# Performance work log

Hardware: AMD Instinct MI355X
Metric: run time of the kernel (lower is better)

## Reference

```python
import jax, jax.numpy as jnp
import numpy as np

B, D, N, H = 2, 1024, 2048, 16
Da = D // H
NEG = -1e30


def setup_inputs() -> dict:
    key = jax.random.key(0)
    k1, k2, k3, k4, k5 = jax.random.split(key, 5)
    x = jax.random.normal(k1, (B, D, N), dtype=jnp.float32)
    mask = jnp.ones((B, N), dtype=jnp.float32)
    s = 1.0 / np.sqrt(D)
    Wq = jax.random.normal(k2, (H, D, Da), dtype=jnp.float32) * s
    Wk = jax.random.normal(k3, (H, D, Da), dtype=jnp.float32) * s
    Wv = jax.random.normal(k4, (H, D, Da), dtype=jnp.float32) * s
    Wo = jax.random.normal(k5, (D, D), dtype=jnp.float32) * s
    return {"x": x, "mask": mask, "Wq": Wq, "Wk": Wk, "Wv": Wv, "Wo": Wo}


def reference(x, mask, Wq, Wk, Wv, Wo):
    # x: [B, D, N] -> [B, N, D]
    xt = jnp.swapaxes(x, 1, 2)
    scale = 1.0 / np.sqrt(Da)
    # per-head projections, batched over heads: [B, H, N, Da]
    q = jnp.einsum("bnd,hde->bhne", xt, Wq)
    k = jnp.einsum("bnd,hde->bhne", xt, Wk)
    v = jnp.einsum("bnd,hde->bhne", xt, Wv)
    # scaled scores: [B, H, N, N]
    scores = jnp.einsum("bhne,bhme->bhnm", q, k) * scale
    hmask = mask[:, None, None, :]  # additive mask over keys
    vmask = mask[:, None, :, None]  # multiplicative mask over queries
    scores = scores * hmask + (1.0 - hmask) * NEG
    attn = jax.nn.softmax(scores, axis=-1) * vmask
    heads = jnp.einsum("bhnm,bhme->bhne", attn, v)
    # concat heads along feature dim: [B, N, H*Da]
    head = jnp.swapaxes(heads, 1, 2).reshape(xt.shape[0], xt.shape[1], H * Da)
    out = head @ Wo  # [B, N, D]
    return jnp.swapaxes(out, 1, 2)  # [B, D, N]
```

## Files before the change

### kernel.cpp

```cpp
#include <hip/hip_runtime.h>

typedef _Float16 f16;
typedef _Float16 f16x4 __attribute__((ext_vector_type(4)));
typedef _Float16 f16x8 __attribute__((ext_vector_type(8)));
typedef __fp16 fp16x2 __attribute__((ext_vector_type(2)));
typedef float f32x4 __attribute__((ext_vector_type(4)));
typedef float f32x16 __attribute__((ext_vector_type(16)));
typedef int i32x4 __attribute__((ext_vector_type(4)));

#define NEGV (-1e30f)

#if __has_builtin(__builtin_amdgcn_exp2f)
#define EXP2(x) __builtin_amdgcn_exp2f(x)
#else
#define EXP2(x) exp2f(x)
#endif

__device__ __forceinline__ void gload16(const f16* g, f16* l) {
  __builtin_amdgcn_global_load_lds(
      (const __attribute__((address_space(1))) void*)g,
      (__attribute__((address_space(3))) void*)l, 16, 0, 0);
}

__device__ __forceinline__ int pkh(float a, float b) {
  fp16x2 p = __builtin_amdgcn_cvt_pkrtz(a, b);
  return __builtin_bit_cast(int, p);
}

__device__ __forceinline__ void plswap(int& a, int& b) {
#if __has_builtin(__builtin_amdgcn_permlane32_swap)
  auto r = __builtin_amdgcn_permlane32_swap(a, b, false, false);
  a = r[0];
  b = r[1];
#else
  int an = __shfl_xor(b, 32);
  int bn = __shfl_xor(a, 32);
  bool lo = (threadIdx.x & 63) < 32;
  int a2 = lo ? a : an;
  int b2 = lo ? bn : b;
  a = a2;
  b = b2;
#endif
}

__global__ __launch_bounds__(256) void prep_kernel(
    const float* __restrict__ x, const float* __restrict__ Wq,
    const float* __restrict__ Wk, const float* __restrict__ Wv,
    const float* __restrict__ Wo, f16* __restrict__ xt,
    f16* __restrict__ WqkvT, f16* __restrict__ WoT)
{
  __shared__ float t[32][33];
  int tx = threadIdx.x & 31, ty = threadIdx.x >> 5;
  int id = blockIdx.x;
  const float* src;
  f16* dst;
  int a0, b0, sld;
  float sc = 1.0f;
  if (id < 4096) {
    int b = id >> 11, rem = id & 2047;
    a0 = (rem >> 6) * 32;
    b0 = (rem & 63) * 32;
    sld = 2048;
    src = x + (size_t)b * 1024 * 2048;
    dst = xt + (size_t)b * 2048 * 1024;
  } else if (id < 7168) {
    int i = id - 4096;
    a0 = (i & 31) * 32;
    b0 = ((i >> 5) & 1) * 32;
    int z = i >> 6, m = z >> 4, h = z & 15;
    sld = 64;
    src = ((m == 0) ? Wq : (m == 1) ? Wk : Wv) + (size_t)h * 65536;
    sc = (m == 0) ? 0.18033688011112042f : 1.0f;
    dst = WqkvT + (size_t)(m * 1024 + h * 64) * 1024;
  } else {
    int i = id - 7168;
    a0 = (i >> 5) * 32;
    b0 = (i & 31) * 32;
    sld = 1024;
    src = Wo;
    dst = WoT;
  }
#pragma unroll
  for (int i = 0; i < 4; ++i)
    t[ty + 8 * i][tx] = src[(size_t)(a0 + ty + 8 * i) * sld + b0 + tx] * sc;
  __syncthreads();
#pragma unroll
  for (int i = 0; i < 4; ++i)
    dst[(size_t)(b0 + ty + 8 * i) * 1024 + a0 + tx] = (f16)t[tx][ty + 8 * i];
}

__global__ __launch_bounds__(512, 4) void gemm_f16_kernel(
    const f16* __restrict__ A, const f16* __restrict__ Bt,
    int K, int ldc, long bstride, long cstride,
    f16* __restrict__ Ch, float* __restrict__ Cf,
    const float* __restrict__ rowmask, int mcol0,
    f16* __restrict__ Vt)
{
  __shared__ __align__(16) f16 smem[8192];
  f16* As = smem;
  f16* Bs = smem + 4096;

  int tid = threadIdx.x;
  int lane = tid & 63, w = tid >> 6, g = lane >> 4, r = lane & 15;
  int wr = w >> 2, wc = w & 3;

  int nbx = gridDim.x;
  int n = nbx * gridDim.y;
  int flat = blockIdx.y * nbx + blockIdx.x;
  int nf = (flat & 7) * (n >> 3) + (flat >> 3);
  int bx = nf % nbx, by = nf / nbx;

  size_t row0 = (size_t)by * 128;
  size_t col0 = (size_t)bx * 128;
  Bt += (size_t)blockIdx.z * (size_t)bstride;

  int srow = lane >> 2;
  int sseg = (lane & 3) * 8;

  f32x4 acc[4][2];
#pragma unroll
  for (int m = 0; m < 4; ++m)
#pragma unroll
    for (int nn = 0; nn < 2; ++nn)
      acc[m][nn] = (f32x4){0.f, 0.f, 0.f, 0.f};

  const f16* Ap = A + (row0 + w * 16 + srow) * (size_t)K + sseg;
  const f16* Bp = Bt + (col0 + w * 16 + srow) * (size_t)K + sseg;

  for (int k0 = 0; k0 < K; k0 += 32) {
    __syncthreads();
    gload16(Ap + k0, As + w * 512);
    gload16(Bp + k0, Bs + w * 512);
    __syncthreads();
    f16x8 af[4], bf[2];
#pragma unroll
    for (int m = 0; m < 4; ++m)
      af[m] = *(const f16x8*)&As[(wr * 64 + m * 16 + r) * 32 + g * 8];
#pragma unroll
    for (int nn = 0; nn < 2; ++nn)
      bf[nn] = *(const f16x8*)&Bs[(wc * 32 + nn * 16 + r) * 32 + g * 8];
#pragma unroll
    for (int m = 0; m < 4; ++m)
#pragma unroll
      for (int nn = 0; nn < 2; ++nn)
        acc[m][nn] = __builtin_amdgcn_mfma_f32_16x16x32_f16(af[m], bf[nn], acc[m][nn], 0, 0, 0);
  }

  if (Vt && col0 >= 2048) {
    int b = (int)(row0 >> 11);
    int n0 = (int)(row0 & 2047);
    int vcol0 = (int)col0 - 2048;
    __syncthreads();
#pragma unroll
    for (int h2 = 0; h2 < 2; ++h2) {
      if ((wc >> 1) == h2) {
        int wcl = wc & 1;
#pragma unroll
        for (int m = 0; m < 4; ++m)
#pragma unroll
          for (int nn = 0; nn < 2; ++nn) {
            int cl = wcl * 32 + nn * 16 + r;
            int row = wr * 64 + m * 16 + g * 4;
            int rowp = row ^ ((cl & 7) << 3);
            f16x4 v4 = {(f16)acc[m][nn][0], (f16)acc[m][nn][1],
                        (f16)acc[m][nn][2], (f16)acc[m][nn][3]};
            *(f16x4*)&smem[cl * 128 + rowp] = v4;
          }
      }
      __syncthreads();
#pragma unroll
      for (int ii = 0; ii < 2; ++ii) {
        int chunk = ii * 512 + tid;
        int el = chunk >> 4, seg = chunk & 15;
        int rowp = (seg * 8) ^ ((el & 7) << 3);
        f16x8 v8 = *(const f16x8*)&smem[el * 128 + rowp];
        *(f16x8*)&Vt[(size_t)(b * 1024 + vcol0 + h2 * 64 + el) * 2048 + n0 + seg * 8] = v8;
      }
      __syncthreads();
    }
  } else if (Ch) {
    Ch += (size_t)blockIdx.z * (size_t)cstride;
#pragma unroll
    for (int m = 0; m < 4; ++m)
#pragma unroll
      for (int nn = 0; nn < 2; ++nn)
#pragma unroll
        for (int q = 0; q < 4; ++q) {
          size_t row = row0 + wr * 64 + m * 16 + g * 4 + q;
          int col = (int)col0 + wc * 32 + nn * 16 + r;
          float v = acc[m][nn][q];
          if (rowmask && col >= mcol0) v *= rowmask[row];
          Ch[row * (size_t)ldc + col] = (f16)v;
        }
  } else {
    Cf += (size_t)blockIdx.z * (size_t)cstride;
#pragma unroll
    for (int m = 0; m < 4; ++m)
#pragma unroll
      for (int nn = 0; nn < 2; ++nn)
#pragma unroll
        for (int q = 0; q < 4; ++q)
          Cf[(row0 + wr * 64 + m * 16 + g * 4 + q) * (size_t)ldc +
             col0 + wc * 32 + nn * 16 + r] = acc[m][nn][q];
  }
}

__global__ __launch_bounds__(512, 4) void attn_kernel(const f16* __restrict__ qk,
                                                      const f16* __restrict__ Vt,
                                                      const float* __restrict__ mask,
                                                      f16* __restrict__ head)
{
  __shared__ __align__(16) f16 smem[16384];
  __shared__ __align__(16) float negc[2048];
  __shared__ __align__(16) float rl[8][32];
  __shared__ __align__(16) float mm[8][32];
  __shared__ __align__(16) float ll[8][32];
  __shared__ __align__(16) float aa[8][32];
  __shared__ __align__(16) float il[4][32];
  __shared__ int aflag;

  int tid = threadIdx.x;
  int w = tid >> 6, lane = tid & 63;
  int l31 = lane & 31, hb = lane >> 5;
  int hb4 = hb * 4;
  int wq = w >> 1, wk = w & 1;

  int flat = blockIdx.x;
  int nf = (flat & 7) * 64 + (flat >> 3);
  int qt = nf & 15, bh = nf >> 4;
  int b = bh >> 4, hh = bh & 15;
  const float* maskb = mask + b * 2048;

  if (tid == 0) aflag = 0;

  int qrow = qt * 128 + wq * 32 + l31;
  const f16* qp = qk + ((size_t)(b * 2048 + qrow)) * 2048 + hh * 64;
  f16x8 qf[4];
#pragma unroll
  for (int ec = 0; ec < 4; ++ec)
    qf[ec] = *(const f16x8*)(qp + ec * 16 + hb * 8);

  const f16* kg0 = qk + ((size_t)(b * 2048)) * 2048 + 1024 + hh * 64;
  const f16* vg0 = Vt + ((size_t)((b * 16 + hh) * 64)) * 2048;

  int srow = tid >> 3;
  int sseg = tid & 7;
  int s2 = (sseg ^ (srow & 7)) * 8;

  auto stage = [&](int nb, int kt_) {
    const f16* kg = kg0 + (size_t)kt_ * 64 * 2048;
    const f16* vg = vg0 + kt_ * 64;
    gload16(kg + (size_t)srow * 2048 + s2, smem + nb * 4096 + w * 512);
    gload16(vg + (size_t)srow * 2048 + s2, smem + 8192 + nb * 4096 + w * 512);
  };

  stage(0, 0);
  __syncthreads();

  {
    const float* mp = maskb + tid * 4;
    f32x4 m0 = *(const f32x4*)(mp);
    int localany = 0;
#pragma unroll
    for (int j = 0; j < 4; ++j) {
      negc[tid * 4 + j] = (1.0f - m0[j]) * NEGV;
      localany |= (m0[j] != 1.0f);
    }
    if (localany) aflag = 1;
  }
  __syncthreads();
  const bool anymask = (aflag != 0);

  f32x16 o0, o1;
#pragma unroll
  for (int i = 0; i < 16; ++i) { o0[i] = 0.f; o1[i] = 0.f; }
  float mrun = -INFINITY, lrun = 0.f;

  int krow = wk * 32 + l31;
  int kb = krow * 64;
  int k7 = krow & 7;
  int vk7 = l31 & 7;
  int vb0 = l31 * 64, vb1 = vb0 + 2048;

  for (int kt = 0; kt < 32; ++kt) {
    int cur = kt & 1;
    if (kt + 1 < 32) stage(cur ^ 1, kt + 1);

    const f16* Kc = smem + cur * 4096;
    const f16* Vc = smem + 8192 + cur * 4096;

    f32x16 s;
    if (anymask) {
      const float* nb = &negc[kt * 64 + wk * 32];
#pragma unroll
      for (int rr = 0; rr < 4; ++rr) {
        f32x4 cv = *(const f32x4*)&nb[rr * 8 + hb4];
#pragma unroll
        for (int j = 0; j < 4; ++j) s[rr * 4 + j] = cv[j];
      }
    } else {
#pragma unroll
      for (int i = 0; i < 16; ++i) s[i] = 0.f;
    }
    __builtin_amdgcn_s_setprio(1);
#pragma unroll
    for (int ec = 0; ec < 4; ++ec) {
      int so = ((((ec << 1) | hb) ^ k7) << 3);
      f16x8 kf = *(const f16x8*)&Kc[kb + so];
      s = __builtin_amdgcn_mfma_f32_32x32x16_f16(kf, qf[ec], s, 0, 0, 0);
    }
    __builtin_amdgcn_s_setprio(0);

    float a[16];
#pragma unroll
    for (int i = 0; i < 16; ++i) a[i] = s[i];
#pragma unroll
    for (int stp = 8; stp > 0; stp >>= 1)
#pragma unroll
      for (int i = 0; i < stp; ++i) a[i] = fmaxf(a[i], a[i + stp]);
    float pmax = fmaxf(a[0], __shfl_xor(a[0], 32));

    if (!__all(pmax - mrun <= 8.0f)) {
      float mnew = fmaxf(mrun, pmax);
      float resc = EXP2(mrun - mnew);
      mrun = mnew;
      lrun *= resc;
      if (hb == 0) rl[w][l31] = resc;
#pragma unroll
      for (int rr = 0; rr < 4; ++rr) {
        f32x4 rv = *(const f32x4*)&rl[w][rr * 8 + hb4];
#pragma unroll
        for (int j = 0; j < 4; ++j) {
          o0[rr * 4 + j] *= rv[j];
          o1[rr * 4 + j] *= rv[j];
        }
      }
    }

    float p[16];
#pragma unroll
    for (int i = 0; i < 16; ++i) p[i] = EXP2(s[i] - mrun);
    float b2[8];
#pragma unroll
    for (int i = 0; i < 8; ++i) b2[i] = p[i] + p[i + 8];
#pragma unroll
    for (int stp = 4; stp > 0; stp >>= 1)
#pragma unroll
      for (int i = 0; i < stp; ++i) b2[i] += b2[i + stp];
    lrun += b2[0] + __shfl_xor(b2[0], 32);

    __builtin_amdgcn_s_setprio(1);
#pragma unroll
    for (int kc = 0; kc < 2; ++kc) {
      int t0a = pkh(p[kc * 8 + 0], p[kc * 8 + 1]);
      int t0b = pkh(p[kc * 8 + 2], p[kc * 8 + 3]);
      int t1a = pkh(p[kc * 8 + 4], p[kc * 8 + 5]);
      int t1b = pkh(p[kc * 8 + 6], p[kc * 8 + 7]);
      plswap(t0a, t1a);
      plswap(t0b, t1b);
      f16x8 af = __builtin_bit_cast(f16x8, (i32x4){t0a, t0b, t1a, t1b});
      int vs = (((wk * 4 + (kc << 1)) | hb) ^ vk7) << 3;
      f16x8 vf0 = *(const f16x8*)&Vc[vb0 + vs];
      f16x8 vf1 = *(const f16x8*)&Vc[vb1 + vs];
      o0 = __builtin_amdgcn_mfma_f32_32x32x16_f16(af, vf0, o0, 0, 0, 0);
      o1 = __builtin_amdgcn_mfma_f32_32x32x16_f16(af, vf1, o1, 0, 0, 0);
    }
    __builtin_amdgcn_s_setprio(0);

    __syncthreads();
  }

  if (hb == 0) {
    mm[w][l31] = mrun;
    ll[w][l31] = lrun;
  }
  __syncthreads();
  {
    float mo = mm[w ^ 1][l31], lo = ll[w ^ 1][l31];
    float mt = fmaxf(mrun, mo);
    float a_self = EXP2(mrun - mt);
    float a_oth = EXP2(mo - mt);
    float lt = lrun * a_self + lo * a_oth;
    if (hb == 0) {
      aa[w][l31] = a_self;
      if (wk == 0) il[wq][l31] = maskb[qrow] / lt;
    }
  }
#pragma unroll
  for (int rr = 0; rr < 4; ++rr) {
    f32x4 av = *(const f32x4*)&aa[w][rr * 8 + hb4];
#pragma unroll
    for (int j = 0; j < 4; ++j) {
      o0[rr * 4 + j] *= av[j];
      o1[rr * 4 + j] *= av[j];
    }
  }
  float* scr = (float*)smem;
  if (wk == 1) {
    float* sp = scr + wq * 2048;
#pragma unroll
    for (int i = 0; i < 16; ++i) {
      sp[i * 64 + lane] = o0[i];
      sp[(16 + i) * 64 + lane] = o1[i];
    }
  }
  __syncthreads();
  if (wk == 0) {
    float* sp = scr + wq * 2048;
#pragma unroll
    for (int i = 0; i < 16; ++i) {
      o0[i] += sp[i * 64 + lane];
      o1[i] += sp[(16 + i) * 64 + lane];
    }
    f16* hp = head + ((size_t)(b * 2048 + qt * 128 + wq * 32)) * 1024 + hh * 64 + l31;
#pragma unroll
    for (int rr = 0; rr < 4; ++rr) {
      f32x4 iv = *(const f32x4*)&il[wq][rr * 8 + hb4];
#pragma unroll
      for (int j = 0; j < 4; ++j) {
        int crow = j + rr * 8 + hb4;
        hp[(size_t)crow * 1024] = (f16)(o0[rr * 4 + j] * iv[j]);
        hp[(size_t)crow * 1024 + 32] = (f16)(o1[rr * 4 + j] * iv[j]);
      }
    }
  }
}

extern "C" void kernel_launch(void* const* d_in, const int* in_sizes, int n_in,
                              void* d_out, int out_size, void* d_ws, size_t ws_size,
                              hipStream_t stream)
{
  const float* x    = (const float*)d_in[0];
  const float* mask = (const float*)d_in[1];
  const float* Wq   = (const float*)d_in[2];
  const float* Wk   = (const float*)d_in[3];
  const float* Wv   = (const float*)d_in[4];
  const float* Wo   = (const float*)d_in[5];
  float* out = (float*)d_out;

  char* ws = (char*)d_ws;
  f16* xt_head = (f16*)(ws);
  f16* WqkvT   = (f16*)(ws + 8388608);
  f16* WoT     = (f16*)(ws + 14680064);
  f16* qk      = (f16*)(ws + 16777216);
  f16* Vt      = (f16*)(ws + 33554432);

  prep_kernel<<<dim3(8192), 256, 0, stream>>>(x, Wq, Wk, Wv, Wo, xt_head, WqkvT, WoT);

  gemm_f16_kernel<<<dim3(24, 32, 1), 512, 0, stream>>>(
      xt_head, WqkvT, 1024, 2048, 0, 0, qk, nullptr, mask, 1024, Vt);

  attn_kernel<<<dim3(512), 512, 0, stream>>>(qk, Vt, mask, xt_head);

  gemm_f16_kernel<<<dim3(16, 8, 2), 512, 0, stream>>>(
      WoT, xt_head, 1024, 2048, (long)2048 * 1024, (long)1024 * 2048, nullptr, out,
      nullptr, 0, nullptr);
}
```

Before: 132.5 us.

## Double attention key tile to 128 and use narrower tiles for output GEMM

The attention kernel now stages 128 keys per iteration instead of 64, doubling the shared K/V buffers and computing two score tiles per wave before one softmax update. This halves the loop trip count and the block barriers, at the cost of more LDS and registers per block, which can lower occupancy. The output-projection GEMM is templated to a 64-wide column tile, doubling the grid to 512 blocks for better CU coverage. A barrier is added before the final rescale step.

```diff
diff --git a/kernel.cpp b/kernel.cpp
--- a/kernel.cpp
+++ b/kernel.cpp
@@ -89,6 +89,7 @@
     dst[(size_t)(b0 + ty + 8 * i) * 1024 + a0 + tx] = (f16)t[tx][ty + 8 * i];
 }
 
+template <int BN>
 __global__ __launch_bounds__(512, 4) void gemm_f16_kernel(
     const f16* __restrict__ A, const f16* __restrict__ Bt,
     int K, int ldc, long bstride, long cstride,
@@ -96,6 +97,7 @@
     const float* __restrict__ rowmask, int mcol0,
     f16* __restrict__ Vt)
 {
+  const int NACC = BN / 64;
   __shared__ __align__(16) f16 smem[8192];
   f16* As = smem;
   f16* Bs = smem + 4096;
@@ -111,17 +113,17 @@
   int bx = nf % nbx, by = nf / nbx;
 
   size_t row0 = (size_t)by * 128;
-  size_t col0 = (size_t)bx * 128;
+  size_t col0 = (size_t)bx * BN;
   Bt += (size_t)blockIdx.z * (size_t)bstride;
 
   int srow = lane >> 2;
   int sseg = (lane & 3) * 8;
 
-  f32x4 acc[4][2];
+  f32x4 acc[4][NACC];
 #pragma unroll
   for (int m = 0; m < 4; ++m)
 #pragma unroll
-    for (int nn = 0; nn < 2; ++nn)
+    for (int nn = 0; nn < NACC; ++nn)
       acc[m][nn] = (f32x4){0.f, 0.f, 0.f, 0.f};
 
   const f16* Ap = A + (row0 + w * 16 + srow) * (size_t)K + sseg;
@@ -130,23 +132,23 @@
   for (int k0 = 0; k0 < K; k0 += 32) {
     __syncthreads();
     gload16(Ap + k0, As + w * 512);
-    gload16(Bp + k0, Bs + w * 512);
+    if (BN == 128 || w < 4) gload16(Bp + k0, Bs + w * 512);
     __syncthreads();
-    f16x8 af[4], bf[2];
+    f16x8 af[4], bf[NACC];
 #pragma unroll
     for (int m = 0; m < 4; ++m)
       af[m] = *(const f16x8*)&As[(wr * 64 + m * 16 + r) * 32 + g * 8];
 #pragma unroll
-    for (int nn = 0; nn < 2; ++nn)
-      bf[nn] = *(const f16x8*)&Bs[(wc * 32 + nn * 16 + r) * 32 + g * 8];
+    for (int nn = 0; nn < NACC; ++nn)
+      bf[nn] = *(const f16x8*)&Bs[(wc * (16 * NACC) + nn * 16 + r) * 32 + g * 8];
 #pragma unroll
     for (int m = 0; m < 4; ++m)
 #pragma unroll
-      for (int nn = 0; nn < 2; ++nn)
+      for (int nn = 0; nn < NACC; ++nn)
         acc[m][nn] = __builtin_amdgcn_mfma_f32_16x16x32_f16(af[m], bf[nn], acc[m][nn], 0, 0, 0);
   }
 
-  if (Vt && col0 >= 2048) {
+  if (BN == 128 && Vt && col0 >= 2048) {
     int b = (int)(row0 >> 11);
     int n0 = (int)(row0 & 2047);
     int vcol0 = (int)col0 - 2048;
@@ -158,7 +160,7 @@
 #pragma unroll
         for (int m = 0; m < 4; ++m)
 #pragma unroll
-          for (int nn = 0; nn < 2; ++nn) {
+          for (int nn = 0; nn < NACC; ++nn) {
             int cl = wcl * 32 + nn * 16 + r;
             int row = wr * 64 + m * 16 + g * 4;
             int rowp = row ^ ((cl & 7) << 3);
@@ -183,11 +185,11 @@
 #pragma unroll
     for (int m = 0; m < 4; ++m)
 #pragma unroll
-      for (int nn = 0; nn < 2; ++nn)
+      for (int nn = 0; nn < NACC; ++nn)
 #pragma unroll
         for (int q = 0; q < 4; ++q) {
           size_t row = row0 + wr * 64 + m * 16 + g * 4 + q;
-          int col = (int)col0 + wc * 32 + nn * 16 + r;
+          int col = (int)col0 + wc * (16 * NACC) + nn * 16 + r;
           float v = acc[m][nn][q];
           if (rowmask && col >= mcol0) v *= rowmask[row];
           Ch[row * (size_t)ldc + col] = (f16)v;
@@ -197,11 +199,11 @@
 #pragma unroll
     for (int m = 0; m < 4; ++m)
 #pragma unroll
-      for (int nn = 0; nn < 2; ++nn)
+      for (int nn = 0; nn < NACC; ++nn)
 #pragma unroll
         for (int q = 0; q < 4; ++q)
           Cf[(row0 + wr * 64 + m * 16 + g * 4 + q) * (size_t)ldc +
-             col0 + wc * 32 + nn * 16 + r] = acc[m][nn][q];
+             col0 + wc * (16 * NACC) + nn * 16 + r] = acc[m][nn][q];
   }
 }
 
@@ -210,7 +212,7 @@
                                                       const float* __restrict__ mask,
                                                       f16* __restrict__ head)
 {
-  __shared__ __align__(16) f16 smem[16384];
+  __shared__ __align__(16) f16 smem[32768];
   __shared__ __align__(16) float negc[2048];
   __shared__ __align__(16) float rl[8][32];
   __shared__ __align__(16) float mm[8][32];
@@ -243,15 +245,20 @@
   const f16* kg0 = qk + ((size_t)(b * 2048)) * 2048 + 1024 + hh * 64;
   const f16* vg0 = Vt + ((size_t)((b * 16 + hh) * 64)) * 2048;
 
-  int srow = tid >> 3;
-  int sseg = tid & 7;
-  int s2 = (sseg ^ (srow & 7)) * 8;
+  int ksrow = tid >> 3, kseg = tid & 7;
+  int ks2 = (kseg ^ (ksrow & 7)) * 8;
+  int vsrow = tid >> 4, vseg2 = tid & 15;
+  int vs2 = (vseg2 ^ (vsrow & 7)) * 8;
 
   auto stage = [&](int nb, int kt_) {
-    const f16* kg = kg0 + (size_t)kt_ * 64 * 2048;
-    const f16* vg = vg0 + kt_ * 64;
-    gload16(kg + (size_t)srow * 2048 + s2, smem + nb * 4096 + w * 512);
-    gload16(vg + (size_t)srow * 2048 + s2, smem + 8192 + nb * 4096 + w * 512);
+    const f16* kg = kg0 + (size_t)kt_ * 128 * 2048;
+    const f16* vg = vg0 + kt_ * 128;
+    f16* Kd = smem + nb * 8192;
+    f16* Vd = smem + 16384 + nb * 8192;
+    gload16(kg + (size_t)ksrow * 2048 + ks2, Kd + w * 512);
+    gload16(kg + (size_t)(ksrow + 64) * 2048 + ks2, Kd + 4096 + w * 512);
+    gload16(vg + (size_t)vsrow * 2048 + vs2, Vd + w * 512);
+    gload16(vg + (size_t)(vsrow + 32) * 2048 + vs2, Vd + 4096 + w * 512);
   };
 
   stage(0, 0);
@@ -276,44 +283,49 @@
   for (int i = 0; i < 16; ++i) { o0[i] = 0.f; o1[i] = 0.f; }
   float mrun = -INFINITY, lrun = 0.f;
 
-  int krow = wk * 32 + l31;
-  int kb = krow * 64;
-  int k7 = krow & 7;
-  int vk7 = l31 & 7;
-  int vb0 = l31 * 64, vb1 = vb0 + 2048;
-
-  for (int kt = 0; kt < 32; ++kt) {
+  int kb0 = (wk * 64 + l31) * 64;
+  int kb1 = kb0 + 2048;
+  int k7 = l31 & 7;
+  int vb0 = l31 * 128, vb1 = vb0 + 4096;
+
+  for (int kt = 0; kt < 16; ++kt) {
     int cur = kt & 1;
-    if (kt + 1 < 32) stage(cur ^ 1, kt + 1);
-
-    const f16* Kc = smem + cur * 4096;
-    const f16* Vc = smem + 8192 + cur * 4096;
-
-    f32x16 s;
+    if (kt + 1 < 16) stage(cur ^ 1, kt + 1);
+
+    const f16* Kc = smem + cur * 8192;
+    const f16* Vc = smem + 16384 + cur * 8192;
+
+    f32x16 s0, s1;
     if (anymask) {
-      const float* nb = &negc[kt * 64 + wk * 32];
+      const float* nb = &negc[kt * 128 + wk * 64];
 #pragma unroll
       for (int rr = 0; rr < 4; ++rr) {
-        f32x4 cv = *(const f32x4*)&nb[rr * 8 + hb4];
-#pragma unroll
-        for (int j = 0; j < 4; ++j) s[rr * 4 + j] = cv[j];
+        f32x4 c0 = *(const f32x4*)&nb[rr * 8 + hb4];
+        f32x4 c1 = *(const f32x4*)&nb[32 + rr * 8 + hb4];
+#pragma unroll
+        for (int j = 0; j < 4; ++j) {
+          s0[rr * 4 + j] = c0[j];
+          s1[rr * 4 + j] = c1[j];
+        }
       }
     } else {
 #pragma unroll
-      for (int i = 0; i < 16; ++i) s[i] = 0.f;
+      for (int i = 0; i < 16; ++i) { s0[i] = 0.f; s1[i] = 0.f; }
     }
     __builtin_amdgcn_s_setprio(1);
 #pragma unroll
     for (int ec = 0; ec < 4; ++ec) {
       int so = ((((ec << 1) | hb) ^ k7) << 3);
-      f16x8 kf = *(const f16x8*)&Kc[kb + so];
-      s = __builtin_amdgcn_mfma_f32_32x32x16_f16(kf, qf[ec], s, 0, 0, 0);
+      f16x8 kf0 = *(const f16x8*)&Kc[kb0 + so];
+      f16x8 kf1 = *(const f16x8*)&Kc[kb1 + so];
+      s0 = __builtin_amdgcn_mfma_f32_32x32x16_f16(kf0, qf[ec], s0, 0, 0, 0);
+      s1 = __builtin_amdgcn_mfma_f32_32x32x16_f16(kf1, qf[ec], s1, 0, 0, 0);
     }
     __builtin_amdgcn_s_setprio(0);
 
     float a[16];
 #pragma unroll
-    for (int i = 0; i < 16; ++i) a[i] = s[i];
+    for (int i = 0; i < 16; ++i) a[i] = fmaxf(s0[i], s1[i]);
 #pragma unroll
     for (int stp = 8; stp > 0; stp >>= 1)
 #pragma unroll
@@ -337,34 +349,40 @@
       }
     }
 
-    float p[16];
-#pragma unroll
-    for (int i = 0; i < 16; ++i) p[i] = EXP2(s[i] - mrun);
-    float b2[8];
-#pragma unroll
-    for (int i = 0; i < 8; ++i) b2[i] = p[i] + p[i + 8];
-#pragma unroll
-    for (int stp = 4; stp > 0; stp >>= 1)
+    float p[2][16];
+#pragma unroll
+    for (int i = 0; i < 16; ++i) {
+      p[0][i] = EXP2(s0[i] - mrun);
+      p[1][i] = EXP2(s1[i] - mrun);
+    }
+    float b2[16];
+#pragma unroll
+    for (int i = 0; i < 16; ++i) b2[i] = p[0][i] + p[1][i];
+#pragma unroll
+    for (int stp = 8; stp > 0; stp >>= 1)
 #pragma unroll
       for (int i = 0; i < stp; ++i) b2[i] += b2[i + stp];
     lrun += b2[0] + __shfl_xor(b2[0], 32);
 
     __builtin_amdgcn_s_setprio(1);
 #pragma unroll
-    for (int kc = 0; kc < 2; ++kc) {
-      int t0a = pkh(p[kc * 8 + 0], p[kc * 8 + 1]);
-      int t0b = pkh(p[kc * 8 + 2], p[kc * 8 + 3]);
-      int t1a = pkh(p[kc * 8 + 4], p[kc * 8 + 5]);
-      int t1b = pkh(p[kc * 8 + 6], p[kc * 8 + 7]);
-      plswap(t0a, t1a);
-      plswap(t0b, t1b);
-      f16x8 af = __builtin_bit_cast(f16x8, (i32x4){t0a, t0b, t1a, t1b});
-      int vs = (((wk * 4 + (kc << 1)) | hb) ^ vk7) << 3;
-      f16x8 vf0 = *(const f16x8*)&Vc[vb0 + vs];
-      f16x8 vf1 = *(const f16x8*)&Vc[vb1 + vs];
-      o0 = __builtin_amdgcn_mfma_f32_32x32x16_f16(af, vf0, o0, 0, 0, 0);
-      o1 = __builtin_amdgcn_mfma_f32_32x32x16_f16(af, vf1, o1, 0, 0, 0);
-    }
+    for (int t = 0; t < 2; ++t)
+#pragma unroll
+      for (int kc = 0; kc < 2; ++kc) {
+        int t0a = pkh(p[t][kc * 8 + 0], p[t][kc * 8 + 1]);
+        int t0b = pkh(p[t][kc * 8 + 2], p[t][kc * 8 + 3]);
+        int t1a = pkh(p[t][kc * 8 + 4], p[t][kc * 8 + 5]);
+        int t1b = pkh(p[t][kc * 8 + 6], p[t][kc * 8 + 7]);
+        plswap(t0a, t1a);
+        plswap(t0b, t1b);
+        f16x8 af = __builtin_bit_cast(f16x8, (i32x4){t0a, t0b, t1a, t1b});
+        int vseg = wk * 8 + t * 4 + kc * 2 + hb;
+        int vs = ((vseg ^ k7) << 3);
+        f16x8 vf0 = *(const f16x8*)&Vc[vb0 + vs];
+        f16x8 vf1 = *(const f16x8*)&Vc[vb1 + vs];
+        o0 = __builtin_amdgcn_mfma_f32_32x32x16_f16(af, vf0, o0, 0, 0, 0);
+        o1 = __builtin_amdgcn_mfma_f32_32x32x16_f16(af, vf1, o1, 0, 0, 0);
+      }
     __builtin_amdgcn_s_setprio(0);
 
     __syncthreads();
@@ -386,6 +404,7 @@
       if (wk == 0) il[wq][l31] = maskb[qrow] / lt;
     }
   }
+  __syncthreads();
 #pragma unroll
   for (int rr = 0; rr < 4; ++rr) {
     f32x4 av = *(const f32x4*)&aa[w][rr * 8 + hb4];
@@ -447,12 +466,12 @@
 
   prep_kernel<<<dim3(8192), 256, 0, stream>>>(x, Wq, Wk, Wv, Wo, xt_head, WqkvT, WoT);
 
-  gemm_f16_kernel<<<dim3(24, 32, 1), 512, 0, stream>>>(
+  gemm_f16_kernel<128><<<dim3(24, 32, 1), 512, 0, stream>>>(
       xt_head, WqkvT, 1024, 2048, 0, 0, qk, nullptr, mask, 1024, Vt);
 
   attn_kernel<<<dim3(512), 512, 0, stream>>>(qk, Vt, mask, xt_head);
 
-  gemm_f16_kernel<<<dim3(16, 8, 2), 512, 0, stream>>>(
+  gemm_f16_kernel<64><<<dim3(32, 8, 2), 512, 0, stream>>>(
       WoT, xt_head, 1024, 2048, (long)2048 * 1024, (long)1024 * 2048, nullptr, out,
       nullptr, 0, nullptr);
 }
```

After: 129.3 us. -2.4%, faster.
